# Optimization experiments

Hardware: AMD Instinct MI355X
Metric: run time of the kernel (lower is better)

The kernel has to match this reference:

```python
import jax, jax.numpy as jnp
import numpy as np

GROUPS = 8
EPS = 1e-5


def setup_inputs() -> dict:
    key = jax.random.key(0)
    ks = jax.random.split(key, 7)
    b, c, h, w = 32, 256, 32, 32
    x = jax.random.normal(ks[0], (b, c, h, w), dtype=jnp.float32)
    gn_weight = jax.random.normal(ks[1], (c,), dtype=jnp.float32) * 0.02 + 1.0
    gn_bias = jax.random.normal(ks[2], (c,), dtype=jnp.float32) * 0.02
    w_qkv = jax.random.normal(ks[3], (3 * c, c), dtype=jnp.float32) / np.sqrt(c)
    b_qkv = jax.random.normal(ks[4], (3 * c,), dtype=jnp.float32) * 0.01
    w_out = jax.random.normal(ks[5], (c, c), dtype=jnp.float32) / np.sqrt(c)
    b_out = jax.random.normal(ks[6], (c,), dtype=jnp.float32) * 0.01
    return {"x": x, "gn_weight": gn_weight, "gn_bias": gn_bias,
            "w_qkv": w_qkv, "b_qkv": b_qkv, "w_out": w_out, "b_out": b_out}


def group_norm(x, weight, bias):
    b, c, h, w = x.shape
    xg = x.reshape(b, GROUPS, c // GROUPS, h, w)
    mean = jnp.mean(xg, axis=(2, 3, 4), keepdims=True)
    var = jnp.var(xg, axis=(2, 3, 4), keepdims=True)
    xg = (xg - mean) * jax.lax.rsqrt(var + EPS)
    x = xg.reshape(b, c, h, w)
    return x * weight[None, :, None, None] + bias[None, :, None, None]


def reference(x, gn_weight, gn_bias, w_qkv, b_qkv, w_out, b_out):
    b, c, h, w = x.shape
    x_norm = group_norm(x, gn_weight, gn_bias)
    # 1x1 conv == channel matmul: (b, 3c, h, w)
    qkv = jnp.einsum('oc,bchw->bohw', w_qkv, x_norm) + b_qkv[None, :, None, None]
    q, k, v = jnp.split(qkv, 3, axis=1)
    hw = h * w
    q = q.reshape(b, c, hw)  # used transposed: (b, hw, c)
    k = k.reshape(b, c, hw)
    v = v.reshape(b, c, hw)
    scale = 1.0 / jnp.sqrt(jnp.float32(c))
    attn = jax.nn.softmax(jnp.einsum('bcs,bct->bst', q, k) * scale, axis=-1)  # (b, hw, hw)
    out = jnp.einsum('bst,bct->bcs', attn, v).reshape(b, c, h, w)
    out = jnp.einsum('oc,bchw->bohw', w_out, out) + b_out[None, :, None, None]
    return out + x
```

## Files before the change

### kernel.cpp

```cpp
#include <hip/hip_runtime.h>
#include <hip/hip_bf16.h>


typedef __bf16 bf16x8 __attribute__((ext_vector_type(8)));
typedef __bf16 bf16x4 __attribute__((ext_vector_type(4)));
typedef __bf16 bf16x2 __attribute__((ext_vector_type(2)));
typedef float f32x4 __attribute__((ext_vector_type(4)));
typedef float f32x16 __attribute__((ext_vector_type(16)));

#define MFMA16(a, b, c) __builtin_amdgcn_mfma_f32_16x16x32_bf16(a, b, c, 0, 0, 0)
#define MFMA32(a, b, c) __builtin_amdgcn_mfma_f32_32x32x16_bf16(a, b, c, 0, 0, 0)

__global__ __launch_bounds__(512) void gn_kernel(const float* __restrict__ x,
                                                 const float* __restrict__ gw,
                                                 const float* __restrict__ gb,
                                                 __bf16* __restrict__ xnT,
                                                 const float* __restrict__ wqkv,
                                                 const float* __restrict__ wout,
                                                 __bf16* __restrict__ wbf) {
    __shared__ float red[16];
    __shared__ float stats[2];
    __shared__ __bf16 Lds[512][40];
    const int b = blockIdx.x >> 3, g = blockIdx.x & 7;
    const size_t base = ((size_t)b * 256 + g * 32) * 1024;
    const float* xp = x + base;
    const int t = threadIdx.x;

    {
        int widx = (blockIdx.x * 512 + t) * 2;
        const float* wsrc = (widx < 196608) ? (wqkv + widx) : (wout + (widx - 196608));
        float2 wv = *(const float2*)wsrc;
        bf16x2 wo;
        wo[0] = (__bf16)wv.x; wo[1] = (__bf16)wv.y;
        *(bf16x2*)&wbf[widx] = wo;
    }

    float s = 0.f, s2 = 0.f;
    #pragma unroll
    for (int i = 0; i < 8; i++) {
        int j = i * 512 + t;
        float4 v0 = *(const float4*)(xp + (size_t)j * 8);
        float4 v1 = *(const float4*)(xp + (size_t)j * 8 + 4);
        s  += v0.x + v0.y + v0.z + v0.w + v1.x + v1.y + v1.z + v1.w;
        s2 += v0.x*v0.x + v0.y*v0.y + v0.z*v0.z + v0.w*v0.w
            + v1.x*v1.x + v1.y*v1.y + v1.z*v1.z + v1.w*v1.w;
    }
    #pragma unroll
    for (int o = 32; o > 0; o >>= 1) { s += __shfl_down(s, o, 64); s2 += __shfl_down(s2, o, 64); }
    const int wv = t >> 6;
    if ((t & 63) == 0) { red[wv * 2] = s; red[wv * 2 + 1] = s2; }
    __syncthreads();
    if (t == 0) {
        float ts = 0.f, ts2 = 0.f;
        for (int w = 0; w < 8; w++) { ts += red[w * 2]; ts2 += red[w * 2 + 1]; }
        float mean = ts / 32768.f;
        float var = ts2 / 32768.f - mean * mean;
        stats[0] = mean; stats[1] = rsqrtf(var + 1e-5f);
    }
    __syncthreads();
    const float mean = stats[0], inv = stats[1];

    const int c = t >> 4;
    const int so = (t & 15) * 2;
    const float ga = gw[g * 32 + c], be = gb[g * 32 + c];

    for (int chunk = 0; chunk < 1024; chunk += 512) {
        #pragma unroll
        for (int i = 0; i < 16; i++) {
            int sl = so + i * 32;
            float2 v = *(const float2*)(xp + (size_t)c * 1024 + chunk + sl);
            Lds[sl][c]     = (__bf16)((v.x - mean) * inv * ga + be);
            Lds[sl + 1][c] = (__bf16)((v.y - mean) * inv * ga + be);
        }
        __syncthreads();
        {
            int sl = t;
            #pragma unroll
            for (int u = 0; u < 4; u++) {
                bf16x8 vv = *(const bf16x8*)&Lds[sl][u * 8];
                *(bf16x8*)&xnT[((size_t)b * 1024 + chunk + sl) * 256 + g * 32 + u * 8] = vv;
            }
        }
        __syncthreads();
    }
}

#define GEMM64_BODY(ArowBase_, BrowBase_)                                               \
    f32x4 acc[4][4] = {};                                                               \
    const int r_ = t >> 1, kc_ = (t & 1) * 32;                                          \
    bf16x8 pa[4], pb[4];                                                                \
    _Pragma("unroll")                                                                   \
    for (int u = 0; u < 4; u++) {                                                       \
        pa[u] = *(const bf16x8*)&(ArowBase_)[(size_t)r_ * 256 + kc_ + u * 8];           \
        pb[u] = *(const bf16x8*)&(BrowBase_)[(size_t)r_ * 256 + kc_ + u * 8];           \
    }                                                                                   \
    for (int kk = 0; kk < 256; kk += 64) {                                              \
        _Pragma("unroll")                                                               \
        for (int u = 0; u < 4; u++) {                                                   \
            *(bf16x8*)&As[r_][kc_ + u * 8] = pa[u];                                     \
            *(bf16x8*)&Bs[r_][kc_ + u * 8] = pb[u];                                     \
        }                                                                               \
        __syncthreads();                                                                \
        if (kk < 192) {                                                                 \
            _Pragma("unroll")                                                           \
            for (int u = 0; u < 4; u++) {                                               \
                pa[u] = *(const bf16x8*)&(ArowBase_)[(size_t)r_ * 256 + kk + 64 + kc_ + u * 8]; \
                pb[u] = *(const bf16x8*)&(BrowBase_)[(size_t)r_ * 256 + kk + 64 + kc_ + u * 8]; \
            }                                                                           \
        }                                                                               \
        _Pragma("unroll")                                                               \
        for (int kh = 0; kh < 2; kh++) {                                                \
            bf16x8 af[4], bfv[4];                                                       \
            _Pragma("unroll")                                                           \
            for (int im = 0; im < 4; im++)                                              \
                af[im] = *(const bf16x8*)&As[wm + im * 16 + l16][kh * 32 + quad * 8];   \
            _Pragma("unroll")                                                           \
            for (int in = 0; in < 4; in++)                                              \
                bfv[in] = *(const bf16x8*)&Bs[wn + in * 16 + l16][kh * 32 + quad * 8];  \
            _Pragma("unroll")                                                           \
            for (int im = 0; im < 4; im++)                                              \
                _Pragma("unroll")                                                       \
                for (int in = 0; in < 4; in++)                                          \
                    acc[im][in] = MFMA16(af[im], bfv[in], acc[im][in]);                 \
        }                                                                               \
        __syncthreads();                                                                \
    }

__global__ __launch_bounds__(256) void qkv_gemm(const __bf16* __restrict__ wbf,
                                                const float* __restrict__ bias,
                                                const __bf16* __restrict__ xnT,
                                                __bf16* __restrict__ qtr,
                                                __bf16* __restrict__ ktr,
                                                __bf16* __restrict__ vbuf) {
    __shared__ union {
        struct { __bf16 A[128][72]; __bf16 B[128][72]; } g;
        __bf16 ct[128][136];
    } sm;
    const int b = blockIdx.z;
    const int n0 = blockIdx.x * 128, m0 = blockIdx.y * 128;
    const int t = threadIdx.x;
    const int wave = t >> 6, lane = t & 63, quad = lane >> 4, l16 = lane & 15;
    const int wm = (wave & 1) * 64, wn = (wave >> 1) * 64;
    const __bf16* arow = wbf + (size_t)m0 * 256;
    const __bf16* brow = xnT + ((size_t)b * 1024 + n0) * 256;
    auto As = sm.g.A;
    auto Bs = sm.g.B;

    GEMM64_BODY(arow, brow)

    if (m0 < 512) {
        #pragma unroll
        for (int im = 0; im < 4; im++) {
            #pragma unroll
            for (int in = 0; in < 4; in++) {
                int ob = m0 + wm + im * 16 + quad * 4;
                bf16x4 ov;
                #pragma unroll
                for (int r = 0; r < 4; r++) ov[r] = (__bf16)(acc[im][in][r] + bias[ob + r]);
                *(bf16x4*)&sm.ct[wn + in * 16 + l16][wm + im * 16 + quad * 4] = ov;
            }
        }
        __syncthreads();
        {
            const int rbase = t >> 2, cf = t & 3;
            #pragma unroll
            for (int rr = 0; rr < 2; rr++) {
                int row = rbase + rr * 64;
                int sg = n0 + row;
                __bf16* dst = (m0 < 256) ? &qtr[((size_t)b * 1024 + sg) * 256 + m0]
                                         : &ktr[((size_t)b * 1024 + sg) * 256 + (m0 - 256)];
                #pragma unroll
                for (int u = 0; u < 4; u++) {
                    int colb = cf * 8 + u * 32;
                    *(bf16x8*)&dst[colb] = *(const bf16x8*)&sm.ct[row][colb];
                }
            }
        }
    } else {
        #pragma unroll
        for (int im = 0; im < 4; im++) {
            #pragma unroll
            for (int in = 0; in < 4; in++) {
                int sg = n0 + wn + in * 16 + l16;
                int ob = m0 + wm + im * 16 + quad * 4;
                #pragma unroll
                for (int r = 0; r < 4; r++) {
                    float val = acc[im][in][r] + bias[ob + r];
                    vbuf[((size_t)b * 256 + (ob - 512 + r)) * 1024 + sg] = (__bf16)val;
                }
            }
        }
    }
}

__global__ __launch_bounds__(512, 2) void attn_kernel(const __bf16* __restrict__ qtr,
                                                      const __bf16* __restrict__ ktr,
                                                      const __bf16* __restrict__ vbuf,
                                                      __bf16* __restrict__ aoT) {
    __shared__ __bf16 Kt[2][32][260];
    __shared__ __bf16 Vs[2][256][36];
    __shared__ __bf16 Pl[4][32][72];
    __shared__ float Lred[4][2][32];
    const int b = blockIdx.x;
    const int tid = threadIdx.x;
    const int wave = tid >> 6, lane = tid & 63, half = lane >> 5, l31 = lane & 31;
    const int pair = wave & 3, th = wave >> 2;
    const int s0 = blockIdx.y * 128 + pair * 32;
    const float kscale = 0.09016844f;

    bf16x8 aq[16];
    #pragma unroll
    for (int ks = 0; ks < 16; ks++)
        aq[ks] = *(const bf16x8*)&qtr[((size_t)b * 1024 + s0 + l31) * 256 + ks * 16 + half * 8];

    const int k_row = tid >> 3;
    const int k_cb  = (tid & 7) * 8;
    const int v_c   = tid >> 1;
    const int v_th  = tid & 1;
    const size_t kbase = (size_t)b * 1024 * 256;
    const size_t vbase = (size_t)b * 256 * 1024;

    float l_part[16] = {};
    f32x16 o_acc[4] = {};

    bf16x8 kpre[4], vpre[4];
    #pragma unroll
    for (int u = 0; u < 4; u++) {
        kpre[u] = *(const bf16x8*)&ktr[kbase + (size_t)k_row * 256 + k_cb + u * 64];
        vpre[u] = *(const bf16x8*)&vbuf[vbase + (size_t)v_c * 1024 + v_th * 32 + u * 8];
    }

    for (int it = 0; it < 16; it++) {
        #pragma unroll
        for (int u = 0; u < 4; u++) {
            *(bf16x8*)&Kt[k_row >> 5][k_row & 31][k_cb + u * 64] = kpre[u];
            *(bf16x8*)&Vs[v_th][v_c][u * 8] = vpre[u];
        }
        __syncthreads();
        if (it < 15) {
            const int t1 = (it + 1) * 64;
            #pragma unroll
            for (int u = 0; u < 4; u++) {
                kpre[u] = *(const bf16x8*)&ktr[kbase + (size_t)(t1 + k_row) * 256 + k_cb + u * 64];
                vpre[u] = *(const bf16x8*)&vbuf[vbase + (size_t)v_c * 1024 + t1 + v_th * 32 + u * 8];
            }
        }

        f32x16 sc_a = {}, sc_b = {};
        __builtin_amdgcn_s_setprio(1);
        #pragma unroll
        for (int ks = 0; ks < 8; ks++) {
            bf16x8 bk0 = *(const bf16x8*)&Kt[th][l31][ks * 16 + half * 8];
            bf16x8 bk1 = *(const bf16x8*)&Kt[th][l31][(ks + 8) * 16 + half * 8];
            sc_a = MFMA32(aq[ks], bk0, sc_a);
            sc_b = MFMA32(aq[ks + 8], bk1, sc_b);
        }
        __builtin_amdgcn_s_setprio(0);
        #pragma unroll
        for (int r = 0; r < 16; r++) {
            float p = exp2f((sc_a[r] + sc_b[r]) * kscale);
            l_part[r] += p;
            int row = (r & 3) + 8 * (r >> 2) + 4 * half;
            Pl[pair][row][th * 32 + l31] = (__bf16)p;
        }
        __syncthreads();

        bf16x8 ap[4];
        #pragma unroll
        for (int kc = 0; kc < 4; kc++)
            ap[kc] = *(const bf16x8*)&Pl[pair][l31][kc * 16 + half * 8];
        __builtin_amdgcn_s_setprio(1);
        #pragma unroll
        for (int n = 0; n < 4; n++) {
            int c = th * 128 + n * 32 + l31;
            #pragma unroll
            for (int kc = 0; kc < 4; kc++) {
                bf16x8 bv = *(const bf16x8*)&Vs[kc >> 1][c][(kc & 1) * 16 + half * 8];
                o_acc[n] = MFMA32(ap[kc], bv, o_acc[n]);
            }
        }
        __builtin_amdgcn_s_setprio(0);
        __syncthreads();
    }

    float lsum[16];
    #pragma unroll
    for (int r = 0; r < 16; r++) {
        float l = l_part[r];
        #pragma unroll
        for (int m = 16; m > 0; m >>= 1) l += __shfl_xor(l, m, 32);
        lsum[r] = l;
        if (l31 == 0) {
            int row = (r & 3) + 8 * (r >> 2) + 4 * half;
            Lred[pair][th][row] = l;
        }
    }
    __syncthreads();
    #pragma unroll
    for (int r = 0; r < 16; r++) {
        int row = (r & 3) + 8 * (r >> 2) + 4 * half;
        float rinv = 1.0f / (lsum[r] + Lred[pair][1 - th][row]);
        #pragma unroll
        for (int n = 0; n < 4; n++) {
            int c = th * 128 + n * 32 + l31;
            aoT[((size_t)b * 1024 + s0 + row) * 256 + c] = (__bf16)(o_acc[n][r] * rinv);
        }
    }
}

__global__ __launch_bounds__(256) void proj_gemm(const __bf16* __restrict__ wbf_out,
                                                 const float* __restrict__ bias,
                                                 const __bf16* __restrict__ aoT,
                                                 const float* __restrict__ resid,
                                                 float* __restrict__ Out) {
    __shared__ union {
        struct { __bf16 A[128][72]; __bf16 B[128][72]; } g;
        float cf[64][132];
    } sm;
    const int b = blockIdx.z;
    const int n0 = blockIdx.x * 128, m0 = blockIdx.y * 128;
    const int t = threadIdx.x;
    const int wave = t >> 6, lane = t & 63, quad = lane >> 4, l16 = lane & 15;
    const int wm = (wave & 1) * 64, wn = (wave >> 1) * 64;
    const __bf16* arow = wbf_out + (size_t)m0 * 256;
    const __bf16* brow = aoT + ((size_t)b * 1024 + n0) * 256;
    auto As = sm.g.A;
    auto Bs = sm.g.B;

    GEMM64_BODY(arow, brow)

    for (int h = 0; h < 2; h++) {
        if ((wave & 1) == h) {
            #pragma unroll
            for (int im = 0; im < 4; im++)
                #pragma unroll
                for (int in = 0; in < 4; in++)
                    #pragma unroll
                    for (int r = 0; r < 4; r++)
                        sm.cf[im * 16 + quad * 4 + r][wn + in * 16 + l16] = acc[im][in][r];
        }
        __syncthreads();
        {
            const int rloc = t >> 2, cq = (t & 3) * 4;
            const int o = m0 + h * 64 + rloc;
            const float bo = bias[o];
            const float* rrow = &resid[((size_t)b * 256 + o) * 1024 + n0];
            float* orow = &Out[((size_t)b * 256 + o) * 1024 + n0];
            #pragma unroll
            for (int u = 0; u < 8; u++) {
                int col = cq + u * 16;
                f32x4 cv = *(const f32x4*)&sm.cf[rloc][col];
                float4 rv = *(const float4*)&rrow[col];
                float4 ov;
                ov.x = cv[0] + bo + rv.x;
                ov.y = cv[1] + bo + rv.y;
                ov.z = cv[2] + bo + rv.z;
                ov.w = cv[3] + bo + rv.w;
                *(float4*)&orow[col] = ov;
            }
        }
        __syncthreads();
    }
}

extern "C" void kernel_launch(void* const* d_in, const int* in_sizes, int n_in,
                              void* d_out, int out_size, void* d_ws, size_t ws_size,
                              hipStream_t stream) {
    const float* x    = (const float*)d_in[0];
    const float* gw   = (const float*)d_in[1];
    const float* gb   = (const float*)d_in[2];
    const float* wqkv = (const float*)d_in[3];
    const float* bqkv = (const float*)d_in[4];
    const float* wout = (const float*)d_in[5];
    const float* bout = (const float*)d_in[6];
    float* out = (float*)d_out;

    const size_t T16 = (size_t)32 * 1024 * 256;
    __bf16* xnT  = (__bf16*)d_ws;
    __bf16* qtr  = xnT + T16;
    __bf16* ktr  = qtr + T16;
    __bf16* vbuf = ktr + T16;
    __bf16* aoT  = vbuf + T16;
    __bf16* wbf  = aoT + T16;

    gn_kernel<<<dim3(256), 512, 0, stream>>>(x, gw, gb, xnT, wqkv, wout, wbf);
    qkv_gemm<<<dim3(8, 6, 32), 256, 0, stream>>>(wbf, bqkv, xnT, qtr, ktr, vbuf);
    attn_kernel<<<dim3(32, 8), 512, 0, stream>>>(qtr, ktr, vbuf, aoT);
    proj_gemm<<<dim3(8, 2, 32), 256, 0, stream>>>(wbf + 196608, bout, aoT, x, out);
}
```

Before: 194.2 us.

## Transpose QK MFMA so P stays in registers, and coalesce V stores via LDS

The QK^T MFMA now swaps its operands, so each lane holds scores for one query row across keys. P can then serve directly as the A operand of the PV MFMA, with only a half-tile exchange between the two wave halves through LDS. V's LDS layout is permuted to match the new k ordering, and the row-sum reduction collapses to one shuffle. Separately, the QKV GEMM epilogue for V stages results in shared memory and writes coalesced 16-byte vectors instead of scattered bf16 stores. The risk is an operand-order or permutation mismatch, and the extra sync in the GEMM epilogue.

```diff
diff --git a/kernel.cpp b/kernel.cpp
--- a/kernel.cpp
+++ b/kernel.cpp
@@ -181,14 +181,21 @@
         for (int im = 0; im < 4; im++) {
             #pragma unroll
             for (int in = 0; in < 4; in++) {
-                int sg = n0 + wn + in * 16 + l16;
-                int ob = m0 + wm + im * 16 + quad * 4;
+                int cl = wm + im * 16 + quad * 4;
+                int tl = wn + in * 16 + l16;
                 #pragma unroll
-                for (int r = 0; r < 4; r++) {
-                    float val = acc[im][in][r] + bias[ob + r];
-                    vbuf[((size_t)b * 256 + (ob - 512 + r)) * 1024 + sg] = (__bf16)val;
-                }
-            }
+                for (int r = 0; r < 4; r++)
+                    sm.ct[cl + r][tl] = (__bf16)(acc[im][in][r] + bias[m0 + cl + r]);
+            }
+        }
+        __syncthreads();
+        {
+            const int row = t >> 1, tc = (t & 1) * 64;
+            const int cglob = m0 - 512 + row;
+            __bf16* dst = &vbuf[((size_t)b * 256 + cglob) * 1024 + n0 + tc];
+            #pragma unroll
+            for (int u = 0; u < 8; u++)
+                *(bf16x8*)&dst[u * 8] = *(const bf16x8*)&sm.ct[row][tc + u * 8];
         }
     }
 }
@@ -199,7 +206,7 @@
                                                       __bf16* __restrict__ aoT) {
     __shared__ __bf16 Kt[2][32][260];
     __shared__ __bf16 Vs[2][256][36];
-    __shared__ __bf16 Pl[4][32][72];
+    __shared__ bf16x8 Pl[4][2][2][64];
     __shared__ float Lred[4][2][32];
     const int b = blockIdx.x;
     const int tid = threadIdx.x;
@@ -220,7 +227,7 @@
     const size_t kbase = (size_t)b * 1024 * 256;
     const size_t vbase = (size_t)b * 256 * 1024;
 
-    float l_part[16] = {};
+    float l_acc = 0.f;
     f32x16 o_acc[4] = {};
 
     bf16x8 kpre[4], vpre[4];
@@ -232,9 +239,14 @@
 
     for (int it = 0; it < 16; it++) {
         #pragma unroll
+        for (int u = 0; u < 4; u++)
+            *(bf16x8*)&Kt[k_row >> 5][k_row & 31][k_cb + u * 64] = kpre[u];
+        #pragma unroll
         for (int u = 0; u < 4; u++) {
-            *(bf16x8*)&Kt[k_row >> 5][k_row & 31][k_cb + u * 64] = kpre[u];
-            *(bf16x8*)&Vs[v_th][v_c][u * 8] = vpre[u];
+            const bf16x4* hv = (const bf16x4*)&vpre[u];
+            const int sbase = (u >> 1) * 16 + (u & 1) * 4;
+            *(bf16x4*)&Vs[v_th][v_c][sbase]     = hv[0];
+            *(bf16x4*)&Vs[v_th][v_c][sbase + 8] = hv[1];
         }
         __syncthreads();
         if (it < 15) {
@@ -252,23 +264,34 @@
         for (int ks = 0; ks < 8; ks++) {
             bf16x8 bk0 = *(const bf16x8*)&Kt[th][l31][ks * 16 + half * 8];
             bf16x8 bk1 = *(const bf16x8*)&Kt[th][l31][(ks + 8) * 16 + half * 8];
-            sc_a = MFMA32(aq[ks], bk0, sc_a);
-            sc_b = MFMA32(aq[ks + 8], bk1, sc_b);
+            sc_a = MFMA32(bk0, aq[ks], sc_a);
+            sc_b = MFMA32(bk1, aq[ks + 8], sc_b);
         }
         __builtin_amdgcn_s_setprio(0);
-        #pragma unroll
-        for (int r = 0; r < 16; r++) {
+
+        bf16x8 pf0, pf1;
+        #pragma unroll
+        for (int r = 0; r < 8; r++) {
             float p = exp2f((sc_a[r] + sc_b[r]) * kscale);
-            l_part[r] += p;
-            int row = (r & 3) + 8 * (r >> 2) + 4 * half;
-            Pl[pair][row][th * 32 + l31] = (__bf16)p;
-        }
-        __syncthreads();
+            l_acc += p;
+            pf0[r] = (__bf16)p;
+        }
+        #pragma unroll
+        for (int r = 8; r < 16; r++) {
+            float p = exp2f((sc_a[r] + sc_b[r]) * kscale);
+            l_acc += p;
+            pf1[r - 8] = (__bf16)p;
+        }
+        Pl[pair][th][0][lane] = pf0;
+        Pl[pair][th][1][lane] = pf1;
+        __syncthreads();
+        bf16x8 pp0 = Pl[pair][1 - th][0][lane];
+        bf16x8 pp1 = Pl[pair][1 - th][1][lane];
 
         bf16x8 ap[4];
-        #pragma unroll
-        for (int kc = 0; kc < 4; kc++)
-            ap[kc] = *(const bf16x8*)&Pl[pair][l31][kc * 16 + half * 8];
+        if (th == 0) { ap[0] = pf0; ap[1] = pf1; ap[2] = pp0; ap[3] = pp1; }
+        else         { ap[0] = pp0; ap[1] = pp1; ap[2] = pf0; ap[3] = pf1; }
+
         __builtin_amdgcn_s_setprio(1);
         #pragma unroll
         for (int n = 0; n < 4; n++) {
@@ -283,23 +306,13 @@
         __syncthreads();
     }
 
-    float lsum[16];
-    #pragma unroll
-    for (int r = 0; r < 16; r++) {
-        float l = l_part[r];
-        #pragma unroll
-        for (int m = 16; m > 0; m >>= 1) l += __shfl_xor(l, m, 32);
-        lsum[r] = l;
-        if (l31 == 0) {
-            int row = (r & 3) + 8 * (r >> 2) + 4 * half;
-            Lred[pair][th][row] = l;
-        }
-    }
+    l_acc += __shfl_xor(l_acc, 32, 64);
+    if (lane < 32) Lred[pair][th][l31] = l_acc;
     __syncthreads();
     #pragma unroll
     for (int r = 0; r < 16; r++) {
         int row = (r & 3) + 8 * (r >> 2) + 4 * half;
-        float rinv = 1.0f / (lsum[r] + Lred[pair][1 - th][row]);
+        float rinv = 1.0f / (Lred[pair][0][row] + Lred[pair][1][row]);
         #pragma unroll
         for (int n = 0; n < 4; n++) {
             int c = th * 128 + n * 32 + l31;
```

Result: no change. 192.1 us (-1.1%).
